# Optimization experiments

Hardware: AMD Instinct MI355X
Metric: run time of the kernel (lower is better)

The kernel has to match this reference:

```python
import jax, jax.numpy as jnp
import numpy as np

SATURATION = 1.0


def setup_inputs() -> dict:
    key = jax.random.key(0)
    k1, k2, k3, k4, k5 = jax.random.split(key, 5)
    B, Q, C = 128, 2048, 8
    L, K = 256, 64
    ts = jax.random.normal(k1, (B, Q, C), dtype=jnp.float32)
    shapelets = jax.random.normal(k2, (L, K, C), dtype=jnp.float32)  # stacked ParameterList
    gating = jax.random.normal(k3, (L,), dtype=jnp.float32)
    fc1_w = jax.random.normal(k4, (2, L), dtype=jnp.float32) / np.sqrt(L)
    fc1_b = jax.random.normal(k5, (2,), dtype=jnp.float32) * 0.01
    return {"ts": ts, "shapelets": shapelets, "gating": gating,
            "fc1_w": fc1_w, "fc1_b": fc1_b}


def reference(ts, shapelets, gating, fc1_w, fc1_b):
    # ts: [B, Q, C]; shapelets: [L, K, C]
    ts = ts.astype(jnp.float32)
    L, K, C = shapelets.shape
    # ||segment||^2 summed over (K, C) via sliding-window cumsum trick -> [B, S]
    ts2 = jnp.sum(ts * ts, axis=2)                     # [B, Q]
    csum = jnp.pad(jnp.cumsum(ts2, axis=1), ((0, 0), (1, 0)))
    win_sq = csum[:, K:] - csum[:, :-K]                # [B, S], S = Q-K+1
    # cross term <segment, shapelet> for all windows/shapelets via 1D conv
    kernel = jnp.transpose(shapelets, (1, 2, 0))       # [K, C, L] (WIO)
    cross = jax.lax.conv_general_dilated(
        ts, kernel, window_strides=(1,), padding='VALID',
        dimension_numbers=('NWC', 'WIO', 'NWC'))       # [B, S, L]
    sh_sq = jnp.sum(shapelets * shapelets, axis=(1, 2))  # [L]
    # mean squared distance per (batch, window, shapelet)
    dist = (win_sq[:, :, None] - 2.0 * cross + sh_sq[None, None, :]) / (K * C)
    hard_min = jnp.min(dist, axis=1)                   # [B, L] min-pool over windows
    g = jax.nn.sigmoid(SATURATION * gating)            # [L]
    min_dw = hard_min * g                              # equivalent to result @ diag(g)
    return min_dw @ fc1_w.T + fc1_b                    # [B, 2]
```

## Files before the change

### kernel.cpp

```cpp
#include <hip/hip_runtime.h>
#include <stdint.h>

#define B_ 128
#define Q_ 2048
#define C_ 8
#define L_ 256
#define K_ 64
#define S_ 1985
#define KC_ 512
#define BNC_ 64
#define NNT_ 4

typedef short s16x8 __attribute__((ext_vector_type(8)));
typedef float f32x16 __attribute__((ext_vector_type(16)));

__device__ __forceinline__ unsigned short f2bf(float f) {
    unsigned u = __float_as_uint(f);
    u += 0x7FFFu + ((u >> 16) & 1u);
    return (unsigned short)(u >> 16);
}
__device__ __forceinline__ unsigned fenc(float f) {
    unsigned u = __float_as_uint(f);
    return (u & 0x80000000u) ? ~u : (u | 0x80000000u);
}
__device__ __forceinline__ float fdec(unsigned k) {
    unsigned u = (k & 0x80000000u) ? (k ^ 0x80000000u) : ~k;
    return __uint_as_float(u);
}
__device__ __forceinline__ void async_copy16(void* lds_dst, const void* g_src) {
    __builtin_amdgcn_global_load_lds(
        (const __attribute__((address_space(1))) void*)g_src,
        (__attribute__((address_space(3))) void*)lds_dst, 16, 0, 0);
}

__global__ __launch_bounds__(256) void k_cast_ts(const float* __restrict__ ts,
                                                 uint4* __restrict__ out) {
    int i = blockIdx.x * 256 + threadIdx.x;
    const float4* p = (const float4*)ts + (size_t)i * 2;
    float4 x = p[0], y = p[1];
    union { unsigned short h[8]; uint4 v; } u;
    u.h[0] = f2bf(x.x); u.h[1] = f2bf(x.y); u.h[2] = f2bf(x.z); u.h[3] = f2bf(x.w);
    u.h[4] = f2bf(y.x); u.h[5] = f2bf(y.y); u.h[6] = f2bf(y.z); u.h[7] = f2bf(y.w);
    out[i] = u.v;
}

__global__ __launch_bounds__(256) void k_pad(uint4* __restrict__ tsb) {
    uint4 z; z.x = z.y = z.z = z.w = 0u;
    tsb[B_ * Q_ + blockIdx.x * 256 + threadIdx.x] = z;
}

__global__ __launch_bounds__(64) void k_prep_sh(const float* __restrict__ sh,
                                                uint4* __restrict__ shb,
                                                float* __restrict__ shsq) {
    const int l = blockIdx.x;
    const int t = threadIdx.x;
    const float4* p = (const float4*)(sh + (size_t)l * KC_) + t * 2;
    float4 x = p[0], y = p[1];
    union { unsigned short h[8]; uint4 v; } u;
    u.h[0] = f2bf(x.x); u.h[1] = f2bf(x.y); u.h[2] = f2bf(x.z); u.h[3] = f2bf(x.w);
    u.h[4] = f2bf(y.x); u.h[5] = f2bf(y.y); u.h[6] = f2bf(y.z); u.h[7] = f2bf(y.w);
    shb[l * 64 + t] = u.v;
    float ss = x.x*x.x + x.y*x.y + x.z*x.z + x.w*x.w
             + y.x*y.x + y.y*y.y + y.z*y.z + y.w*y.w;
    #pragma unroll
    for (int off = 32; off >= 1; off >>= 1) ss += __shfl_down(ss, off, 64);
    if (t == 0) shsq[l] = ss;
}

__global__ __launch_bounds__(256) void k_wq(const float* __restrict__ ts,
                                            float* __restrict__ wqg) {
    const int b = blockIdx.x;
    const int t = threadIdx.x;
    __shared__ float t2[2048];
    #pragma unroll
    for (int j = 0; j < 8; ++j) {
        int r = j * 256 + t;
        const float4* p = (const float4*)(ts + ((size_t)b * Q_ + r) * C_);
        float4 x = p[0], y = p[1];
        t2[r] = x.x*x.x + x.y*x.y + x.z*x.z + x.w*x.w
              + y.x*y.x + y.y*y.y + y.z*y.z + y.w*y.w;
    }
    __syncthreads();
    const float inf = __builtin_inff();
    int s0 = t * 8;
    float w = 0.f;
    if (s0 < S_) {
        #pragma unroll 16
        for (int k = 0; k < K_; ++k) w += t2[s0 + k];
    }
    #pragma unroll
    for (int j = 0; j < 8; ++j) {
        int s = s0 + j;
        wqg[(size_t)b * Q_ + s] = (s < S_) ? w : inf;
        if (s + 1 < S_) w = w + t2[s + K_] - t2[s];
    }
}

__global__ __launch_bounds__(256) void k_init(unsigned* __restrict__ hmin) {
    hmin[blockIdx.x * 256 + threadIdx.x] = 0xFFFFFFFFu;
}

__global__ __launch_bounds__(256, 2) void k_main(
    const uint4* __restrict__ tsb,
    const char*  __restrict__ shb,
    const float* __restrict__ wqg,
    const float* __restrict__ shsq,
    unsigned*    __restrict__ hmin)
{
    __shared__ uint4 b_lds4[4096];
    __shared__ uint4 a_lds4[2][320];
    __shared__ float wqt[2][256];

    const int nt   = blockIdx.x;
    const int b    = blockIdx.y;
    const int c0   = nt * BNC_;
    const int tid  = threadIdx.x;
    const int lane = tid & 63;
    const int wv   = tid >> 6;
    const int l31  = lane & 31;
    const int hi   = lane >> 5;

    #define STAGE_A(p, mi_)                                                    \
        {                                                                      \
            const char* gA = (const char*)(tsb + (size_t)b * Q_ + (mi_) * 256);\
            async_copy16((char*)&a_lds4[p][wv * 64] + lane * 16,               \
                         gA + (wv * 64 + lane) * 16);                          \
            if (wv == 0)                                                       \
                async_copy16((char*)&a_lds4[p][256] + lane * 16,               \
                             gA + (256 + lane) * 16);                          \
            else if (wv == 1)                                                  \
                async_copy16((char*)&wqt[p][0] + lane * 16,                    \
                             (const char*)(wqg + (size_t)b * Q_ + (mi_) * 256) \
                             + lane * 16);                                     \
        }

    #pragma unroll
    for (int it = 0; it < 16; ++it) {
        int col  = wv * 16 + it;
        const char* g = shb + ((size_t)(c0 + col)) * 1024
                      + ((lane ^ (col & 31)) << 4);
        async_copy16((char*)b_lds4 + col * 1024, g);
    }
    STAGE_A(0, 0)
    __syncthreads();

    const f32x16 fz = {0.f,0.f,0.f,0.f,0.f,0.f,0.f,0.f,
                       0.f,0.f,0.f,0.f,0.f,0.f,0.f,0.f};
    const float inf = __builtin_inff();
    float rm0 = inf, rm1 = inf;

    const char* bb    = (const char*)b_lds4;
    const int   abase = (wv * 64 + l31 + hi) * 16;
    const int   bcol  = l31 * 1024;

    #pragma unroll 1
    for (int mi = 0; mi < 8; ++mi) {
        const int p = mi & 1;
        if (mi < 7) STAGE_A(p ^ 1, mi + 1)

        f32x16 acc00 = fz, acc01 = fz;
        f32x16 acc10 = fz, acc11 = fz;
        const char* ab = (const char*)&a_lds4[p][0];
        #pragma unroll
        for (int kk = 0; kk < 32; ++kk) {
            s16x8 a0 = *(const s16x8*)(ab + abase + kk * 32);
            s16x8 a1 = *(const s16x8*)(ab + abase + kk * 32 + 512);
            int ch = (((kk << 1) + hi) ^ l31) << 4;
            s16x8 b0 = *(const s16x8*)(bb + bcol + ch);
            s16x8 b1 = *(const s16x8*)(bb + bcol + ch + 32768);
            __builtin_amdgcn_s_setprio(1);
            acc00 = __builtin_amdgcn_mfma_f32_32x32x16_bf16(a0, b0, acc00, 0, 0, 0);
            acc01 = __builtin_amdgcn_mfma_f32_32x32x16_bf16(a0, b1, acc01, 0, 0, 0);
            acc10 = __builtin_amdgcn_mfma_f32_32x32x16_bf16(a1, b0, acc10, 0, 0, 0);
            acc11 = __builtin_amdgcn_mfma_f32_32x32x16_bf16(a1, b1, acc11, 0, 0, 0);
            __builtin_amdgcn_s_setprio(0);
        }

        {
            int rb = wv * 64 + 4 * hi;
            #pragma unroll
            for (int r = 0; r < 16; ++r) {
                int row = rb + (r & 3) + 8 * (r >> 2);
                float w0 = wqt[p][row];
                float w1 = wqt[p][row + 32];
                rm0 = fminf(rm0, fminf(w0 - 2.f * acc00[r], w1 - 2.f * acc10[r]));
                rm1 = fminf(rm1, fminf(w0 - 2.f * acc01[r], w1 - 2.f * acc11[r]));
            }
        }
        __syncthreads();
    }

    const int colg = c0 + l31;
    rm0 = (rm0 + shsq[colg])      * (1.f / 512.f);
    rm1 = (rm1 + shsq[colg + 32]) * (1.f / 512.f);
    rm0 = fminf(rm0, __shfl_xor(rm0, 32, 64));
    rm1 = fminf(rm1, __shfl_xor(rm1, 32, 64));
    if (hi == 0) {
        atomicMin(&hmin[b * L_ + colg],      fenc(rm0));
        atomicMin(&hmin[b * L_ + colg + 32], fenc(rm1));
    }
}

__global__ __launch_bounds__(256) void k_final(const unsigned* __restrict__ hmin,
                                               const float* __restrict__ gating,
                                               const float* __restrict__ w,
                                               const float* __restrict__ bias,
                                               float* __restrict__ out) {
    const int b = blockIdx.x, t = threadIdx.x;
    float v = fdec(hmin[b * L_ + t]);
    float g = 1.f / (1.f + __expf(-gating[t]));
    float mg = v * g;
    float p0 = mg * w[t];
    float p1 = mg * w[L_ + t];
    #pragma unroll
    for (int off = 32; off >= 1; off >>= 1) {
        p0 += __shfl_down(p0, off, 64);
        p1 += __shfl_down(p1, off, 64);
    }
    __shared__ float r0[4], r1[4];
    int wvi = t >> 6, ln = t & 63;
    if (ln == 0) { r0[wvi] = p0; r1[wvi] = p1; }
    __syncthreads();
    if (t == 0) {
        out[b * 2 + 0] = r0[0] + r0[1] + r0[2] + r0[3] + bias[0];
        out[b * 2 + 1] = r1[0] + r1[1] + r1[2] + r1[3] + bias[1];
    }
}

extern "C" void kernel_launch(void* const* d_in, const int* in_sizes, int n_in,
                              void* d_out, int out_size, void* d_ws, size_t ws_size,
                              hipStream_t stream) {
    const float* ts     = (const float*)d_in[0];
    const float* sh     = (const float*)d_in[1];
    const float* gating = (const float*)d_in[2];
    const float* fw     = (const float*)d_in[3];
    const float* fb     = (const float*)d_in[4];
    float* out = (float*)d_out;

    char* ws = (char*)d_ws;
    uint4*    tsb  = (uint4*)ws;
    char*     shb  = ws + 4202496;
    float*    shsq = (float*)(ws + 4464640);
    unsigned* hmin = (unsigned*)(ws + 4465664);
    float*    wqg  = (float*)(ws + 4596736);

    k_cast_ts<<<1024, 256, 0, stream>>>(ts, tsb);
    k_pad<<<2, 256, 0, stream>>>(tsb);
    k_prep_sh<<<256, 64, 0, stream>>>(sh, (uint4*)shb, shsq);
    k_wq<<<128, 256, 0, stream>>>(ts, wqg);
    k_init<<<128, 256, 0, stream>>>(hmin);
    dim3 grid(NNT_, B_);
    k_main<<<grid, 256, 0, stream>>>(tsb, shb, wqg, shsq, hmin);
    k_final<<<128, 256, 0, stream>>>(hmin, gating, fw, fb, out);
}
```

Baseline: 72.40 us.

## Fold window norms into MFMA accumulators and merge prep kernels

Merges the ts cast and window-sum kernels into one per-batch prep kernel, and merges the pad and hmin-init kernels, cutting the launch count. The window squared-norm term (-0.5*w, split into hi/lo bf16) is injected into the accumulators with an extra MFMA, so the epilogue becomes a pure min over -2*acc. The main loop now handles 128 rows per wave per iteration (4 iterations instead of 8) with a single A buffer instead of double buffering. That trades the async prefetch overlap and adds register pressure for less epilogue work and fewer barriers. The bf16 hi/lo split may slightly change numerics.

```diff
diff --git a/kernel.cpp b/kernel.cpp
--- a/kernel.cpp
+++ b/kernel.cpp
@@ -33,20 +33,56 @@
         (__attribute__((address_space(3))) void*)lds_dst, 16, 0, 0);
 }
 
-__global__ __launch_bounds__(256) void k_cast_ts(const float* __restrict__ ts,
-                                                 uint4* __restrict__ out) {
-    int i = blockIdx.x * 256 + threadIdx.x;
-    const float4* p = (const float4*)ts + (size_t)i * 2;
-    float4 x = p[0], y = p[1];
-    union { unsigned short h[8]; uint4 v; } u;
-    u.h[0] = f2bf(x.x); u.h[1] = f2bf(x.y); u.h[2] = f2bf(x.z); u.h[3] = f2bf(x.w);
-    u.h[4] = f2bf(y.x); u.h[5] = f2bf(y.y); u.h[6] = f2bf(y.z); u.h[7] = f2bf(y.w);
-    out[i] = u.v;
-}
-
-__global__ __launch_bounds__(256) void k_pad(uint4* __restrict__ tsb) {
-    uint4 z; z.x = z.y = z.z = z.w = 0u;
-    tsb[B_ * Q_ + blockIdx.x * 256 + threadIdx.x] = z;
+__global__ __launch_bounds__(256) void k_prep_ts(const float* __restrict__ ts,
+                                                 uint4* __restrict__ tsb,
+                                                 unsigned* __restrict__ extg) {
+    const int b = blockIdx.x;
+    const int t = threadIdx.x;
+    __shared__ float t2[2048];
+    #pragma unroll
+    for (int j = 0; j < 8; ++j) {
+        int r = j * 256 + t;
+        const float4* p = (const float4*)(ts + ((size_t)b * Q_ + r) * C_);
+        float4 x = p[0], y = p[1];
+        union { unsigned short h[8]; uint4 v; } u;
+        u.h[0] = f2bf(x.x); u.h[1] = f2bf(x.y); u.h[2] = f2bf(x.z); u.h[3] = f2bf(x.w);
+        u.h[4] = f2bf(y.x); u.h[5] = f2bf(y.y); u.h[6] = f2bf(y.z); u.h[7] = f2bf(y.w);
+        tsb[(size_t)b * Q_ + r] = u.v;
+        t2[r] = x.x*x.x + x.y*x.y + x.z*x.z + x.w*x.w
+              + y.x*y.x + y.y*y.y + y.z*y.z + y.w*y.w;
+    }
+    __syncthreads();
+    int s0 = t * 8;
+    float w = 0.f;
+    if (s0 < S_) {
+        #pragma unroll 16
+        for (int k = 0; k < K_; ++k) w += t2[s0 + k];
+    }
+    #pragma unroll
+    for (int j = 0; j < 8; ++j) {
+        int s = s0 + j;
+        unsigned word = 0x0000FF80u;
+        if (s < S_) {
+            float v = -0.5f * w;
+            unsigned short hh = f2bf(v);
+            float hf = __uint_as_float((unsigned)hh << 16);
+            unsigned short ll = f2bf(v - hf);
+            word = (unsigned)hh | ((unsigned)ll << 16);
+        }
+        extg[(size_t)b * Q_ + s] = word;
+        if (s + K_ < Q_) w += t2[s + K_] - t2[s];
+    }
+}
+
+__global__ __launch_bounds__(256) void k_misc(uint4* __restrict__ tsb,
+                                              unsigned* __restrict__ hmin) {
+    const int bid = blockIdx.x, t = threadIdx.x;
+    if (bid < 2) {
+        uint4 z; z.x = z.y = z.z = z.w = 0u;
+        tsb[B_ * Q_ + bid * 256 + t] = z;
+    } else {
+        hmin[(bid - 2) * 256 + t] = 0xFFFFFFFFu;
+    }
 }
 
 __global__ __launch_bounds__(64) void k_prep_sh(const float* __restrict__ sh,
@@ -67,49 +103,16 @@
     if (t == 0) shsq[l] = ss;
 }
 
-__global__ __launch_bounds__(256) void k_wq(const float* __restrict__ ts,
-                                            float* __restrict__ wqg) {
-    const int b = blockIdx.x;
-    const int t = threadIdx.x;
-    __shared__ float t2[2048];
-    #pragma unroll
-    for (int j = 0; j < 8; ++j) {
-        int r = j * 256 + t;
-        const float4* p = (const float4*)(ts + ((size_t)b * Q_ + r) * C_);
-        float4 x = p[0], y = p[1];
-        t2[r] = x.x*x.x + x.y*x.y + x.z*x.z + x.w*x.w
-              + y.x*y.x + y.y*y.y + y.z*y.z + y.w*y.w;
-    }
-    __syncthreads();
-    const float inf = __builtin_inff();
-    int s0 = t * 8;
-    float w = 0.f;
-    if (s0 < S_) {
-        #pragma unroll 16
-        for (int k = 0; k < K_; ++k) w += t2[s0 + k];
-    }
-    #pragma unroll
-    for (int j = 0; j < 8; ++j) {
-        int s = s0 + j;
-        wqg[(size_t)b * Q_ + s] = (s < S_) ? w : inf;
-        if (s + 1 < S_) w = w + t2[s + K_] - t2[s];
-    }
-}
-
-__global__ __launch_bounds__(256) void k_init(unsigned* __restrict__ hmin) {
-    hmin[blockIdx.x * 256 + threadIdx.x] = 0xFFFFFFFFu;
-}
-
 __global__ __launch_bounds__(256, 2) void k_main(
     const uint4* __restrict__ tsb,
     const char*  __restrict__ shb,
-    const float* __restrict__ wqg,
+    const unsigned* __restrict__ extg,
     const float* __restrict__ shsq,
     unsigned*    __restrict__ hmin)
 {
     __shared__ uint4 b_lds4[4096];
-    __shared__ uint4 a_lds4[2][320];
-    __shared__ float wqt[2][256];
+    __shared__ uint4 a_lds4[576];
+    __shared__ uint4 e_lds4[128];
 
     const int nt   = blockIdx.x;
     const int b    = blockIdx.y;
@@ -120,18 +123,15 @@
     const int l31  = lane & 31;
     const int hi   = lane >> 5;
 
-    #define STAGE_A(p, mi_)                                                    \
+    #define STAGE_AE(mi_)                                                      \
         {                                                                      \
-            const char* gA = (const char*)(tsb + (size_t)b * Q_ + (mi_) * 256);\
-            async_copy16((char*)&a_lds4[p][wv * 64] + lane * 16,               \
-                         gA + (wv * 64 + lane) * 16);                          \
-            if (wv == 0)                                                       \
-                async_copy16((char*)&a_lds4[p][256] + lane * 16,               \
-                             gA + (256 + lane) * 16);                          \
-            else if (wv == 1)                                                  \
-                async_copy16((char*)&wqt[p][0] + lane * 16,                    \
-                             (const char*)(wqg + (size_t)b * Q_ + (mi_) * 256) \
-                             + lane * 16);                                     \
+            const char* gA = (const char*)(tsb + (size_t)b * Q_ + (mi_) * 512);\
+            for (int rr = tid; rr < 576; rr += 256)                            \
+                async_copy16((char*)a_lds4 + rr * 16, gA + rr * 16);           \
+            if (tid < 128)                                                     \
+                async_copy16((char*)e_lds4 + tid * 16,                         \
+                             (const char*)(extg + (size_t)b * Q_ + (mi_) * 512)\
+                             + tid * 16);                                      \
         }
 
     #pragma unroll
@@ -141,7 +141,7 @@
                       + ((lane ^ (col & 31)) << 4);
         async_copy16((char*)b_lds4 + col * 1024, g);
     }
-    STAGE_A(0, 0)
+    STAGE_AE(0)
     __syncthreads();
 
     const f32x16 fz = {0.f,0.f,0.f,0.f,0.f,0.f,0.f,0.f,
@@ -150,21 +150,28 @@
     float rm0 = inf, rm1 = inf;
 
     const char* bb    = (const char*)b_lds4;
-    const int   abase = (wv * 64 + l31 + hi) * 16;
+    const char* ab    = (const char*)a_lds4;
+    const char* eb    = (const char*)e_lds4;
+    const int   abase = (wv * 128 + l31 + hi) * 16;
     const int   bcol  = l31 * 1024;
 
+    union UU { unsigned u[4]; s16x8 v; };
+    UU be; be.u[0] = hi ? 0u : 0x3F803F80u;
+    be.u[1] = 0u; be.u[2] = 0u; be.u[3] = 0u;
+
     #pragma unroll 1
-    for (int mi = 0; mi < 8; ++mi) {
-        const int p = mi & 1;
-        if (mi < 7) STAGE_A(p ^ 1, mi + 1)
-
+    for (int mi = 0; mi < 4; ++mi) {
         f32x16 acc00 = fz, acc01 = fz;
         f32x16 acc10 = fz, acc11 = fz;
-        const char* ab = (const char*)&a_lds4[p][0];
+        f32x16 acc20 = fz, acc21 = fz;
+        f32x16 acc30 = fz, acc31 = fz;
+
         #pragma unroll
         for (int kk = 0; kk < 32; ++kk) {
             s16x8 a0 = *(const s16x8*)(ab + abase + kk * 32);
             s16x8 a1 = *(const s16x8*)(ab + abase + kk * 32 + 512);
+            s16x8 a2 = *(const s16x8*)(ab + abase + kk * 32 + 1024);
+            s16x8 a3 = *(const s16x8*)(ab + abase + kk * 32 + 1536);
             int ch = (((kk << 1) + hi) ^ l31) << 4;
             s16x8 b0 = *(const s16x8*)(bb + bcol + ch);
             s16x8 b1 = *(const s16x8*)(bb + bcol + ch + 32768);
@@ -173,20 +180,40 @@
             acc01 = __builtin_amdgcn_mfma_f32_32x32x16_bf16(a0, b1, acc01, 0, 0, 0);
             acc10 = __builtin_amdgcn_mfma_f32_32x32x16_bf16(a1, b0, acc10, 0, 0, 0);
             acc11 = __builtin_amdgcn_mfma_f32_32x32x16_bf16(a1, b1, acc11, 0, 0, 0);
+            acc20 = __builtin_amdgcn_mfma_f32_32x32x16_bf16(a2, b0, acc20, 0, 0, 0);
+            acc21 = __builtin_amdgcn_mfma_f32_32x32x16_bf16(a2, b1, acc21, 0, 0, 0);
+            acc30 = __builtin_amdgcn_mfma_f32_32x32x16_bf16(a3, b0, acc30, 0, 0, 0);
+            acc31 = __builtin_amdgcn_mfma_f32_32x32x16_bf16(a3, b1, acc31, 0, 0, 0);
             __builtin_amdgcn_s_setprio(0);
         }
-
         {
-            int rb = wv * 64 + 4 * hi;
-            #pragma unroll
-            for (int r = 0; r < 16; ++r) {
-                int row = rb + (r & 3) + 8 * (r >> 2);
-                float w0 = wqt[p][row];
-                float w1 = wqt[p][row + 32];
-                rm0 = fminf(rm0, fminf(w0 - 2.f * acc00[r], w1 - 2.f * acc10[r]));
-                rm1 = fminf(rm1, fminf(w0 - 2.f * acc01[r], w1 - 2.f * acc11[r]));
-            }
-        }
+            unsigned w0 = *(const unsigned*)(eb + (wv * 128 +  0 + l31) * 4);
+            unsigned w1 = *(const unsigned*)(eb + (wv * 128 + 32 + l31) * 4);
+            unsigned w2 = *(const unsigned*)(eb + (wv * 128 + 64 + l31) * 4);
+            unsigned w3 = *(const unsigned*)(eb + (wv * 128 + 96 + l31) * 4);
+            UU ae0, ae1, ae2, ae3;
+            ae0.u[0] = hi ? 0u : w0; ae0.u[1] = 0; ae0.u[2] = 0; ae0.u[3] = 0;
+            ae1.u[0] = hi ? 0u : w1; ae1.u[1] = 0; ae1.u[2] = 0; ae1.u[3] = 0;
+            ae2.u[0] = hi ? 0u : w2; ae2.u[1] = 0; ae2.u[2] = 0; ae2.u[3] = 0;
+            ae3.u[0] = hi ? 0u : w3; ae3.u[1] = 0; ae3.u[2] = 0; ae3.u[3] = 0;
+            acc00 = __builtin_amdgcn_mfma_f32_32x32x16_bf16(ae0.v, be.v, acc00, 0, 0, 0);
+            acc01 = __builtin_amdgcn_mfma_f32_32x32x16_bf16(ae0.v, be.v, acc01, 0, 0, 0);
+            acc10 = __builtin_amdgcn_mfma_f32_32x32x16_bf16(ae1.v, be.v, acc10, 0, 0, 0);
+            acc11 = __builtin_amdgcn_mfma_f32_32x32x16_bf16(ae1.v, be.v, acc11, 0, 0, 0);
+            acc20 = __builtin_amdgcn_mfma_f32_32x32x16_bf16(ae2.v, be.v, acc20, 0, 0, 0);
+            acc21 = __builtin_amdgcn_mfma_f32_32x32x16_bf16(ae2.v, be.v, acc21, 0, 0, 0);
+            acc30 = __builtin_amdgcn_mfma_f32_32x32x16_bf16(ae3.v, be.v, acc30, 0, 0, 0);
+            acc31 = __builtin_amdgcn_mfma_f32_32x32x16_bf16(ae3.v, be.v, acc31, 0, 0, 0);
+        }
+        __syncthreads();
+        if (mi < 3) STAGE_AE(mi + 1)
+
+        #define FOLD(accv, rmv)                                                \
+            { _Pragma("unroll") for (int r = 0; r < 16; ++r)                   \
+                  rmv = fminf(rmv, -2.f * accv[r]); }
+        FOLD(acc00, rm0) FOLD(acc10, rm0) FOLD(acc20, rm0) FOLD(acc30, rm0)
+        FOLD(acc01, rm1) FOLD(acc11, rm1) FOLD(acc21, rm1) FOLD(acc31, rm1)
+        #undef FOLD
         __syncthreads();
     }
 
@@ -242,14 +269,12 @@
     char*     shb  = ws + 4202496;
     float*    shsq = (float*)(ws + 4464640);
     unsigned* hmin = (unsigned*)(ws + 4465664);
-    float*    wqg  = (float*)(ws + 4596736);
-
-    k_cast_ts<<<1024, 256, 0, stream>>>(ts, tsb);
-    k_pad<<<2, 256, 0, stream>>>(tsb);
+    unsigned* extg = (unsigned*)(ws + 4596736);
+
+    k_prep_ts<<<128, 256, 0, stream>>>(ts, tsb, extg);
+    k_misc<<<130, 256, 0, stream>>>(tsb, hmin);
     k_prep_sh<<<256, 64, 0, stream>>>(sh, (uint4*)shb, shsq);
-    k_wq<<<128, 256, 0, stream>>>(ts, wqg);
-    k_init<<<128, 256, 0, stream>>>(hmin);
     dim3 grid(NNT_, B_);
-    k_main<<<grid, 256, 0, stream>>>(tsb, shb, wqg, shsq, hmin);
+    k_main<<<grid, 256, 0, stream>>>(tsb, shb, extg, shsq, hmin);
     k_final<<<128, 256, 0, stream>>>(hmin, gating, fw, fb, out);
 }
```

Result: faster. 66.74 us (-7.8%).
